# Kernel optimization log

Measured on AMD Instinct MI355X. Metric: run time of the kernel, lower is better.

Reference implementation:

```python
import jax, jax.numpy as jnp
import numpy as np

N = 100000      # nodes
E = 2500000     # edges
DIN, H, DOUT = 3, 32, 4
EPS = 1e-5

def _lin(k, i, o):
    kw, kb = jax.random.split(k)
    lim = 1.0 / np.sqrt(i)
    W = jax.random.uniform(kw, (i, o), jnp.float32, -lim, lim)
    b = jax.random.uniform(kb, (o,), jnp.float32, -lim, lim)
    return W, b

def setup_inputs():
    key = jax.random.key(0)
    ks = jax.random.split(key, 12)
    x = jax.random.normal(ks[0], (N, DIN), jnp.float32)
    edge_index = jax.random.randint(ks[1], (2, E), 0, N, dtype=jnp.int32)
    w_in1, b_in1 = _lin(ks[2], DIN, H)
    w_in2, b_in2 = _lin(ks[3], H, H)
    gamma = jnp.ones((H,), jnp.float32)
    beta = jnp.zeros((H,), jnp.float32)
    wg1, bg1 = _lin(ks[4], H, H)
    wg2, bg2 = _lin(ks[5], H, H)
    wg3, bg3 = _lin(ks[6], H, H)
    wo1, bo1 = _lin(ks[7], H, H)
    wo2, bo2 = _lin(ks[8], H, H)
    wo3, bo3 = _lin(ks[9], H, DOUT)
    return dict(x=x, w_in1=w_in1, b_in1=b_in1, w_in2=w_in2, b_in2=b_in2,
                gamma=gamma, beta=beta,
                wg1=wg1, bg1=bg1, wg2=wg2, bg2=bg2, wg3=wg3, bg3=bg3,
                wo1=wo1, bo1=bo1, wo2=wo2, bo2=bo2, wo3=wo3, bo3=bo3,
                edge_index=edge_index)

def _gcn(h, W, b, src, dst, norm):
    # PyG GCNConv: x' = scatter_add(norm * (xW)[src] -> dst) + bias
    hw = h @ W                                   # [N, H]
    msg = hw[src] * norm[:, None]                # [E+N, H] gather + scale
    out = jax.ops.segment_sum(msg, dst, num_segments=N)
    return out + b

def reference(x, w_in1, b_in1, w_in2, b_in2, gamma, beta,
              wg1, bg1, wg2, bg2, wg3, bg3,
              wo1, bo1, wo2, bo2, wo3, bo3, edge_index):
    leaky = lambda v: jax.nn.leaky_relu(v, 0.01)
    # input MLP
    h = leaky(x @ w_in1 + b_in1)
    h = leaky(h @ w_in2 + b_in2)
    # BatchNorm1d (training-mode batch statistics, biased variance)
    mu = jnp.mean(h, axis=0)
    var = jnp.mean((h - mu) ** 2, axis=0)
    h = (h - mu) * jax.lax.rsqrt(var + EPS) * gamma + beta
    # gcn_norm with self-loops: deg over target index, sym normalization
    loop = jnp.arange(N, dtype=edge_index.dtype)
    src = jnp.concatenate([edge_index[0], loop])
    dst = jnp.concatenate([edge_index[1], loop])
    deg = jax.ops.segment_sum(jnp.ones_like(src, jnp.float32), dst, num_segments=N)
    dis = jax.lax.rsqrt(deg)                     # deg >= 1 due to self-loops
    norm = dis[src] * dis[dst]                   # [E+N]
    h = jax.nn.elu(_gcn(h, wg1, bg1, src, dst, norm))
    h = jax.nn.elu(_gcn(h, wg2, bg2, src, dst, norm))
    h = jax.nn.elu(_gcn(h, wg3, bg3, src, dst, norm))
    # output MLP
    r = leaky(h @ wo1 + bo1)
    r = leaky(r @ wo2 + bo2)
    r = r @ wo3 + bo3                            # [N, 4]
    r = r.at[:, 0].set(jax.nn.sigmoid(r[:, 0]))
    return r
```

## Files before the change

kernel.cpp:

```cpp
#include <hip/hip_runtime.h>
#include <hip/hip_fp16.h>

#define HF 32
#define EPS 1e-5f
#define BSH 7
#define BSZ 128
#define CH  4096
#define SUBCAP 512
#define CAP (8*SUBCAP)

typedef int vi4 __attribute__((ext_vector_type(4)));

__device__ __forceinline__ float leaky(float v){ return fmaxf(v, 0.01f*v); }
__device__ __forceinline__ float elu1(float v){ return v > 0.f ? v : (expf(v)-1.f); }
__device__ __forceinline__ float sigmoidf(float v){ return 1.f/(1.f+expf(-v)); }

__device__ __forceinline__ int4 nt_load_i4(const int* p){
    vi4 v = __builtin_nontemporal_load((const vi4*)p);
    return make_int4(v.x, v.y, v.z, v.w);
}

__device__ __forceinline__ void addrow8(float* a, float4 v){
    const __half2* p = (const __half2*)&v;
#pragma unroll
    for (int k = 0; k < 4; k++){
        float2 f = __half22float2(p[k]);
        a[2*k] += f.x; a[2*k+1] += f.y;
    }
}
__device__ __forceinline__ float4 h2add4f(float4 a, float4 b){
    __half2* pa = (__half2*)&a; __half2* pb = (__half2*)&b;
    float4 r; __half2* pr = (__half2*)&r;
#pragma unroll
    for (int k = 0; k < 4; k++) pr[k] = __hadd2(pa[k], pb[k]);
    return r;
}

union SMem {
    struct {
        float sW1[3*HF]; float sB1[HF]; float sW2[HF*HF]; float sB2[HF];
        float sh[256][33];
    } mlp;
    struct { int lcnt[1024]; int lbase[1024]; int lpos[1024]; } bin;
};

__global__ __launch_bounds__(256)
void k_mlp_bin(const float* __restrict__ x,
               const float* __restrict__ w1, const float* __restrict__ b1,
               const float* __restrict__ w2, const float* __restrict__ b2,
               __half* __restrict__ h, float* __restrict__ stats,
               const int* __restrict__ src, const int* __restrict__ dst,
               int* __restrict__ gfill, int* __restrict__ ep,
               int N, int E, int B, int NC){
    __shared__ SMem sm;
    int t = threadIdx.x;
    if ((int)blockIdx.x < NC){
        int bid = blockIdx.x;
        for (int i = t; i < B; i += 256){ sm.bin.lcnt[i] = 0; sm.bin.lpos[i] = 0; }
        __syncthreads();
        int base = bid * CH;
        int xcd = bid & 7;
        int dv[16], sv[16];
        if (base + CH <= E){
#pragma unroll
            for (int i = 0; i < 4; i++){
                int4 d4 = nt_load_i4(dst + base + (t + i*256)*4);
                int4 s4 = nt_load_i4(src + base + (t + i*256)*4);
                dv[4*i]   = d4.x; dv[4*i+1] = d4.y; dv[4*i+2] = d4.z; dv[4*i+3] = d4.w;
                sv[4*i]   = s4.x; sv[4*i+1] = s4.y; sv[4*i+2] = s4.z; sv[4*i+3] = s4.w;
            }
        } else {
#pragma unroll
            for (int i = 0; i < 16; i++){
                int e = base + t + i*256;
                dv[i] = (e < E) ? dst[e] : -1;
                sv[i] = (e < E) ? src[e] : 0;
            }
        }
#pragma unroll
        for (int i = 0; i < 16; i++)
            if (dv[i] >= 0) atomicAdd(&sm.bin.lcnt[dv[i] >> BSH], 1);
        __syncthreads();
        for (int i = t; i < B; i += 256){
            int c = sm.bin.lcnt[i];
            sm.bin.lbase[i] = c ? (i*CAP + xcd*SUBCAP + atomicAdd(&gfill[i*8 + xcd], c)) : 0;
        }
        __syncthreads();
#pragma unroll
        for (int i = 0; i < 16; i++)
            if (dv[i] >= 0){
                int bb = dv[i] >> BSH;
                int p = sm.bin.lbase[bb] + atomicAdd(&sm.bin.lpos[bb], 1);
                ep[p] = (sv[i] << BSH) | (dv[i] & (BSZ-1));
            }
    } else {
        for (int i = t; i < 3*HF; i += 256) sm.mlp.sW1[i] = w1[i];
        if (t < HF){ sm.mlp.sB1[t] = b1[t]; sm.mlp.sB2[t] = b2[t]; }
        for (int i = t; i < HF*HF; i += 256) sm.mlp.sW2[i] = w2[i];
        __syncthreads();
        int n = (blockIdx.x - NC)*256 + t;
        float h2[HF];
        if (n < N){
            float x0 = x[(size_t)n*3], x1 = x[(size_t)n*3+1], x2 = x[(size_t)n*3+2];
            float h1[HF];
#pragma unroll
            for (int j = 0; j < HF; j++){
                float v = fmaf(x0, sm.mlp.sW1[j], fmaf(x1, sm.mlp.sW1[HF+j],
                          fmaf(x2, sm.mlp.sW1[2*HF+j], sm.mlp.sB1[j])));
                h1[j] = leaky(v);
            }
#pragma unroll
            for (int j = 0; j < HF; j++){
                float v = sm.mlp.sB2[j];
#pragma unroll
                for (int i = 0; i < HF; i++) v = fmaf(h1[i], sm.mlp.sW2[i*HF+j], v);
                h2[j] = leaky(v);
            }
            float4* hv = (float4*)(h + (size_t)n*HF);
#pragma unroll
            for (int jb = 0; jb < 4; jb++){
                __half2 hh[4];
#pragma unroll
                for (int k = 0; k < 4; k++)
                    hh[k] = __float22half2_rn(make_float2(h2[jb*8+2*k], h2[jb*8+2*k+1]));
                hv[jb] = *(float4*)hh;
            }
        } else {
#pragma unroll
            for (int j = 0; j < HF; j++) h2[j] = 0.f;
        }
#pragma unroll
        for (int j = 0; j < HF; j++) sm.mlp.sh[t][j] = h2[j];
        __syncthreads();
        int f = t & 31, g = t >> 5;
        float s = 0.f, ss = 0.f;
        for (int i = 0; i < 32; i++){
            float v = sm.mlp.sh[g*32 + i][f];
            s += v; ss += v*v;
        }
        __syncthreads();
        sm.mlp.sh[g][f] = s; sm.mlp.sh[8+g][f] = ss;
        __syncthreads();
        if (t < HF){
            float a = 0.f, b = 0.f;
#pragma unroll
            for (int g2 = 0; g2 < 8; g2++){ a += sm.mlp.sh[g2][t]; b += sm.mlp.sh[8+g2][t]; }
            atomicAdd(&stats[t], a);
            atomicAdd(&stats[HF+t], b);
        }
    }
}

__global__ __launch_bounds__(256)
void k_csr_t1(int* __restrict__ ep, const int* __restrict__ gfill,
              int2* __restrict__ rowp2, float* __restrict__ dis,
              int* __restrict__ norder,
              const __half* __restrict__ h, const float* __restrict__ stats,
              const float* __restrict__ gamma, const float* __restrict__ beta,
              const float* __restrict__ W, __half* __restrict__ tout,
              int N, int B){
    __shared__ int sep[CAP];
    __shared__ int lcnt[128], lpre[128], lfill[128];
    __shared__ float sW[HF*HF];
    __shared__ float sscale[HF], sshift[HF];
    int t = threadIdx.x;
    int b = blockIdx.x;
    for (int i = t; i < HF*HF; i += 256) sW[i] = W[i];
    if (t < HF){
        float inv = 1.0f/(float)N;
        float mu  = stats[t]*inv;
        float var = stats[HF+t]*inv - mu*mu;
        float rs  = rsqrtf(var + EPS);
        float sc  = rs*gamma[t];
        sscale[t] = sc;
        sshift[t] = beta[t] - mu*sc;
    }
    if (t < 128){ lcnt[t] = 0; lfill[t] = 0; }
    int cx[8], coff[8], cnt = 0;
#pragma unroll
    for (int xx = 0; xx < 8; xx++){ cx[xx] = gfill[b*8 + xx]; coff[xx] = cnt; cnt += cx[xx]; }
    int base = b*CAP;
    __syncthreads();
#pragma unroll
    for (int xx = 0; xx < 8; xx++)
        for (int j = t; j < cx[xx]; j += 256) sep[coff[xx] + j] = ep[base + xx*SUBCAP + j];
    __syncthreads();
    for (int e = t; e < cnt; e += 256) atomicAdd(&lcnt[sep[e] & (BSZ-1)], 1);
    __syncthreads();
    int dg = 0; float dloc = 0.f; int n = b*BSZ + t;
    if (t < 128){
        dg = lcnt[t];
        int pre = 0, rank = 0;
        for (int j = 0; j < 128; j++){
            int dj = lcnt[j];
            if (j < t) pre += dj;
            if (dj > dg || (dj == dg && j < t)) rank++;
        }
        lpre[t] = pre;
        if (n < N){
            rowp2[n] = make_int2(base + pre, base + pre + dg);
            dloc = rsqrtf((float)dg + 1.0f);
            dis[n] = dloc;
            norder[b*BSZ + rank] = n;
        } else {
            norder[b*BSZ + rank] = -1;
        }
    }
    __syncthreads();
    for (int e = t; e < cnt; e += 256){
        int val = sep[e];
        int d = val & (BSZ-1);
        int p = lpre[d] + atomicAdd(&lfill[d], 1);
        ep[base + p] = val >> BSH;
    }
    if (t < 128 && n < N){
        const float4* hv4 = (const float4*)h + (size_t)n*4;
        float v[HF];
#pragma unroll
        for (int k = 0; k < 4; k++){
            float4 raw = hv4[k];
            const __half2* p2 = (const __half2*)&raw;
#pragma unroll
            for (int q = 0; q < 4; q++){
                float2 f2 = __half22float2(p2[q]);
                v[8*k + 2*q]     = f2.x;
                v[8*k + 2*q + 1] = f2.y;
            }
        }
#pragma unroll
        for (int f = 0; f < HF; f++) v[f] = fmaf(v[f], sscale[f], sshift[f]);
        float o[HF];
#pragma unroll
        for (int j = 0; j < HF; j++) o[j] = 0.f;
#pragma unroll
        for (int i = 0; i < HF; i++){
            float vi = v[i];
#pragma unroll
            for (int j4 = 0; j4 < 8; j4++){
                float4 w4 = *(const float4*)&sW[i*HF + 4*j4];
                o[4*j4]   = fmaf(vi, w4.x, o[4*j4]);
                o[4*j4+1] = fmaf(vi, w4.y, o[4*j4+1]);
                o[4*j4+2] = fmaf(vi, w4.z, o[4*j4+2]);
                o[4*j4+3] = fmaf(vi, w4.w, o[4*j4+3]);
            }
        }
        float4* ov = (float4*)tout + (size_t)n*4;
#pragma unroll
        for (int k = 0; k < 4; k++){
            __half2 hh[4];
#pragma unroll
            for (int q = 0; q < 4; q++)
                hh[q] = __float22half2_rn(make_float2(o[8*k+2*q]*dloc, o[8*k+2*q+1]*dloc));
            ov[k] = *(float4*)hh;
        }
    }
}

__global__ __launch_bounds__(256)
void k_gather_t(const __half* __restrict__ tin, const int* __restrict__ esrc,
                const int2* __restrict__ rowp2, const float* __restrict__ dis,
                const int* __restrict__ norder,
                const float* __restrict__ bias, const float* __restrict__ W,
                __half* __restrict__ tout, int N){
    __shared__ float sW[HF*HF];
    __shared__ float sh[64][33];
    int tid = threadIdx.x;
    for (int i = tid; i < HF*HF; i += 256) sW[i] = W[i];
    int nib = tid >> 2, l = tid & 3;
    int n = norder[blockIdx.x*64 + nib];
    float acc[8] = {0.f,0.f,0.f,0.f,0.f,0.f,0.f,0.f};
    float d = 0.f;
    const float4* tv = (const float4*)tin;
    if (n >= 0){
        addrow8(acc, tv[(size_t)n*4 + l]);
        int2 r = rowp2[n];
        int e = r.x, e1 = r.y;
        while (e < e1 && (e & 3)){ addrow8(acc, tv[(size_t)esrc[e]*4 + l]); e++; }
        for (; e + 7 < e1; e += 8){
            int4 a4 = nt_load_i4(&esrc[e]);
            int4 b4 = nt_load_i4(&esrc[e+4]);
            float4 v0 = tv[(size_t)a4.x*4 + l];
            float4 v1 = tv[(size_t)a4.y*4 + l];
            float4 v2 = tv[(size_t)a4.z*4 + l];
            float4 v3 = tv[(size_t)a4.w*4 + l];
            float4 v4 = tv[(size_t)b4.x*4 + l];
            float4 v5 = tv[(size_t)b4.y*4 + l];
            float4 v6 = tv[(size_t)b4.z*4 + l];
            float4 v7 = tv[(size_t)b4.w*4 + l];
            addrow8(acc, h2add4f(h2add4f(v0, v1), h2add4f(v2, v3)));
            addrow8(acc, h2add4f(h2add4f(v4, v5), h2add4f(v6, v7)));
        }
        for (; e + 3 < e1; e += 4){
            int4 s4 = nt_load_i4(&esrc[e]);
            float4 v0 = tv[(size_t)s4.x*4 + l];
            float4 v1 = tv[(size_t)s4.y*4 + l];
            float4 v2 = tv[(size_t)s4.z*4 + l];
            float4 v3 = tv[(size_t)s4.w*4 + l];
            addrow8(acc, h2add4f(h2add4f(v0, v1), h2add4f(v2, v3)));
        }
        for (; e < e1; e++) addrow8(acc, tv[(size_t)esrc[e]*4 + l]);
        d = dis[n];
#pragma unroll
        for (int c = 0; c < 8; c++)
            acc[c] = elu1(fmaf(d, acc[c], bias[8*l + c]));
    }
    __syncthreads();
#pragma unroll
    for (int c = 0; c < 8; c++) sh[nib][8*l + c] = acc[c];
    __syncthreads();
    float o[8] = {0.f,0.f,0.f,0.f,0.f,0.f,0.f,0.f};
#pragma unroll
    for (int i = 0; i < HF; i++){
        float hvv = sh[nib][i];
        float4 w0 = *(const float4*)&sW[i*HF + 8*l];
        float4 w1 = *(const float4*)&sW[i*HF + 8*l + 4];
        o[0] = fmaf(hvv, w0.x, o[0]); o[1] = fmaf(hvv, w0.y, o[1]);
        o[2] = fmaf(hvv, w0.z, o[2]); o[3] = fmaf(hvv, w0.w, o[3]);
        o[4] = fmaf(hvv, w1.x, o[4]); o[5] = fmaf(hvv, w1.y, o[5]);
        o[6] = fmaf(hvv, w1.z, o[6]); o[7] = fmaf(hvv, w1.w, o[7]);
    }
    if (n >= 0){
        __half2 hh[4];
#pragma unroll
        for (int k = 0; k < 4; k++)
            hh[k] = __float22half2_rn(make_float2(o[2*k]*d, o[2*k+1]*d));
        ((float4*)tout)[(size_t)n*4 + l] = *(float4*)hh;
    }
}

__global__ __launch_bounds__(256)
void k_gather_out(const __half* __restrict__ tin, const int* __restrict__ esrc,
                  const int2* __restrict__ rowp2, const float* __restrict__ dis,
                  const int* __restrict__ norder,
                  const float* __restrict__ bg3,
                  const float* __restrict__ wo1, const float* __restrict__ bo1,
                  const float* __restrict__ wo2, const float* __restrict__ bo2,
                  const float* __restrict__ wo3, const float* __restrict__ bo3,
                  float* __restrict__ out, int N){
    __shared__ float sW1[HF*HF], sW2[HF*HF], sW3[HF*4];
    __shared__ float sh[64][33], sh2[64][33];
    int tid = threadIdx.x;
    for (int i = tid; i < HF*HF; i += 256){ sW1[i] = wo1[i]; sW2[i] = wo2[i]; }
    if (tid < HF*4) sW3[tid] = wo3[tid];
    int nib = tid >> 2, l = tid & 3;
    int n = norder[blockIdx.x*64 + nib];
    float acc[8] = {0.f,0.f,0.f,0.f,0.f,0.f,0.f,0.f};
    const float4* tv = (const float4*)tin;
    if (n >= 0){
        addrow8(acc, tv[(size_t)n*4 + l]);
        int2 r = rowp2[n];
        int e = r.x, e1 = r.y;
        while (e < e1 && (e & 3)){ addrow8(acc, tv[(size_t)esrc[e]*4 + l]); e++; }
        for (; e + 7 < e1; e += 8){
            int4 a4 = nt_load_i4(&esrc[e]);
            int4 b4 = nt_load_i4(&esrc[e+4]);
            float4 v0 = tv[(size_t)a4.x*4 + l];
            float4 v1 = tv[(size_t)a4.y*4 + l];
            float4 v2 = tv[(size_t)a4.z*4 + l];
            float4 v3 = tv[(size_t)a4.w*4 + l];
            float4 v4 = tv[(size_t)b4.x*4 + l];
            float4 v5 = tv[(size_t)b4.y*4 + l];
            float4 v6 = tv[(size_t)b4.z*4 + l];
            float4 v7 = tv[(size_t)b4.w*4 + l];
            addrow8(acc, h2add4f(h2add4f(v0, v1), h2add4f(v2, v3)));
            addrow8(acc, h2add4f(h2add4f(v4, v5), h2add4f(v6, v7)));
        }
        for (; e + 3 < e1; e += 4){
            int4 s4 = nt_load_i4(&esrc[e]);
            float4 v0 = tv[(size_t)s4.x*4 + l];
            float4 v1 = tv[(size_t)s4.y*4 + l];
            float4 v2 = tv[(size_t)s4.z*4 + l];
            float4 v3 = tv[(size_t)s4.w*4 + l];
            addrow8(acc, h2add4f(h2add4f(v0, v1), h2add4f(v2, v3)));
        }
        for (; e < e1; e++) addrow8(acc, tv[(size_t)esrc[e]*4 + l]);
        float d = dis[n];
#pragma unroll
        for (int c = 0; c < 8; c++)
            acc[c] = elu1(fmaf(d, acc[c], bg3[8*l + c]));
    }
    __syncthreads();
#pragma unroll
    for (int c = 0; c < 8; c++) sh[nib][8*l + c] = acc[c];
    __syncthreads();
    float o1[8];
#pragma unroll
    for (int c = 0; c < 8; c++) o1[c] = bo1[8*l + c];
#pragma unroll
    for (int i = 0; i < HF; i++){
        float hvv = sh[nib][i];
        float4 w0 = *(const float4*)&sW1[i*HF + 8*l];
        float4 w1 = *(const float4*)&sW1[i*HF + 8*l + 4];
        o1[0] = fmaf(hvv, w0.x, o1[0]); o1[1] = fmaf(hvv, w0.y, o1[1]);
        o1[2] = fmaf(hvv, w0.z, o1[2]); o1[3] = fmaf(hvv, w0.w, o1[3]);
        o1[4] = fmaf(hvv, w1.x, o1[4]); o1[5] = fmaf(hvv, w1.y, o1[5]);
        o1[6] = fmaf(hvv, w1.z, o1[6]); o1[7] = fmaf(hvv, w1.w, o1[7]);
    }
#pragma unroll
    for (int c = 0; c < 8; c++) sh2[nib][8*l + c] = leaky(o1[c]);
    __syncthreads();
    float o2[8];
#pragma unroll
    for (int c = 0; c < 8; c++) o2[c] = bo2[8*l + c];
#pragma unroll
    for (int i = 0; i < HF; i++){
        float hvv = sh2[nib][i];
        float4 w0 = *(const float4*)&sW2[i*HF + 8*l];
        float4 w1 = *(const float4*)&sW2[i*HF + 8*l + 4];
        o2[0] = fmaf(hvv, w0.x, o2[0]); o2[1] = fmaf(hvv, w0.y, o2[1]);
        o2[2] = fmaf(hvv, w0.z, o2[2]); o2[3] = fmaf(hvv, w0.w, o2[3]);
        o2[4] = fmaf(hvv, w1.x, o2[4]); o2[5] = fmaf(hvv, w1.y, o2[5]);
        o2[6] = fmaf(hvv, w1.z, o2[6]); o2[7] = fmaf(hvv, w1.w, o2[7]);
    }
#pragma unroll
    for (int c = 0; c < 8; c++) sh[nib][8*l + c] = leaky(o2[c]);
    __syncthreads();
    if (n >= 0){
        float v = bo3[l];
#pragma unroll
        for (int i = 0; i < HF; i++) v = fmaf(sh[nib][i], sW3[i*4 + l], v);
        if (l == 0) v = sigmoidf(v);
        out[(size_t)n*4 + l] = v;
    }
}

extern "C" void kernel_launch(void* const* d_in, const int* in_sizes, int n_in,
                              void* d_out, int out_size, void* d_ws, size_t ws_size,
                              hipStream_t stream) {
    const float* x     = (const float*)d_in[0];
    const float* w_in1 = (const float*)d_in[1];
    const float* b_in1 = (const float*)d_in[2];
    const float* w_in2 = (const float*)d_in[3];
    const float* b_in2 = (const float*)d_in[4];
    const float* gamma = (const float*)d_in[5];
    const float* beta  = (const float*)d_in[6];
    const float* wg1   = (const float*)d_in[7];
    const float* bg1   = (const float*)d_in[8];
    const float* wg2   = (const float*)d_in[9];
    const float* bg2   = (const float*)d_in[10];
    const float* wg3   = (const float*)d_in[11];
    const float* bg3   = (const float*)d_in[12];
    const float* wo1   = (const float*)d_in[13];
    const float* bo1   = (const float*)d_in[14];
    const float* wo2   = (const float*)d_in[15];
    const float* bo2   = (const float*)d_in[16];
    const float* wo3   = (const float*)d_in[17];
    const float* bo3   = (const float*)d_in[18];
    const int*   ei    = (const int*)d_in[19];

    int N = in_sizes[0] / 3;
    int E = in_sizes[19] / 2;
    int B = (N + BSZ - 1) >> BSH;

    char* w = (char*)d_ws;
    size_t o = 0;
    auto alloc = [&](size_t bytes){ size_t r = o; o = (o + bytes + 255) & ~(size_t)255; return r; };
    float* stats = (float*)(w + alloc(2*HF*sizeof(float)));
    int*   gfill = (int*)  (w + alloc((size_t)B*8*4));
    size_t zero_bytes = o;
    int2*  rowp2 = (int2*) (w + alloc((size_t)N*8));
    float* dis   = (float*)(w + alloc((size_t)N*4));
    int*   norder= (int*)  (w + alloc((size_t)B*BSZ*4));
    int*   ep    = (int*)  (w + alloc((size_t)B*CAP*4));
    __half* bufH = (__half*)(w + alloc((size_t)N*HF*2));
    __half* tA   = (__half*)(w + alloc((size_t)N*HF*2));
    __half* tB   = (__half*)(w + alloc((size_t)N*HF*2));

    hipMemsetAsync(d_ws, 0, zero_bytes, stream);

    const int* src = ei;
    const int* dst = ei + E;
    int NB1 = (N + 255) / 256;
    int NC  = (E + CH - 1) / CH;
    int NS  = 2*B;

    k_mlp_bin<<<NC + NB1, 256, 0, stream>>>(x, w_in1, b_in1, w_in2, b_in2, bufH, stats,
                                            src, dst, gfill, ep, N, E, B, NC);
    k_csr_t1<<<B, 256, 0, stream>>>(ep, gfill, rowp2, dis, norder,
                                    bufH, stats, gamma, beta, wg1, tA, N, B);
    k_gather_t<<<NS, 256, 0, stream>>>(tA, ep, rowp2, dis, norder, bg1, wg2, tB, N);
    k_gather_t<<<NS, 256, 0, stream>>>(tB, ep, rowp2, dis, norder, bg2, wg3, tA, N);
    k_gather_out<<<NS, 256, 0, stream>>>(tA, ep, rowp2, dis, norder, bg3,
                                         wo1, bo1, wo2, bo2, wo3, bo3, (float*)d_out, N);
}
```

Baseline: 307.4 us.

## Replace degree-sorted node ordering with 8 threads per node split across edge chunks

Removes the per-block degree ranking and norder permutation. The gather kernels now assign 8 threads per node (two halves of 4 lanes each take alternating 4-edge chunks) and combine them with a shuffle-xor reduction, halving nodes per block and doubling the grid. The dense transform work is also split so each lane computes 4 output features, and the first-layer transform in k_csr_t1 uses all 256 threads (two per node) instead of 128. This trades degree-sorted load balancing for more memory-level parallelism per node, but adds a shuffle reduction and an extra barrier.

```diff
diff --git a/kernel.cpp b/kernel.cpp
--- a/kernel.cpp
+++ b/kernel.cpp
@@ -154,7 +154,6 @@
 __global__ __launch_bounds__(256)
 void k_csr_t1(int* __restrict__ ep, const int* __restrict__ gfill,
               int2* __restrict__ rowp2, float* __restrict__ dis,
-              int* __restrict__ norder,
               const __half* __restrict__ h, const float* __restrict__ stats,
               const float* __restrict__ gamma, const float* __restrict__ beta,
               const float* __restrict__ W, __half* __restrict__ tout,
@@ -187,23 +186,15 @@
     __syncthreads();
     for (int e = t; e < cnt; e += 256) atomicAdd(&lcnt[sep[e] & (BSZ-1)], 1);
     __syncthreads();
-    int dg = 0; float dloc = 0.f; int n = b*BSZ + t;
     if (t < 128){
-        dg = lcnt[t];
-        int pre = 0, rank = 0;
-        for (int j = 0; j < 128; j++){
-            int dj = lcnt[j];
-            if (j < t) pre += dj;
-            if (dj > dg || (dj == dg && j < t)) rank++;
-        }
+        int dg = lcnt[t];
+        int pre = 0;
+        for (int j = 0; j < t; j++) pre += lcnt[j];
         lpre[t] = pre;
+        int n = b*BSZ + t;
         if (n < N){
             rowp2[n] = make_int2(base + pre, base + pre + dg);
-            dloc = rsqrtf((float)dg + 1.0f);
-            dis[n] = dloc;
-            norder[b*BSZ + rank] = n;
-        } else {
-            norder[b*BSZ + rank] = -1;
+            dis[n]   = rsqrtf((float)dg + 1.0f);
         }
     }
     __syncthreads();
@@ -213,7 +204,10 @@
         int p = lpre[d] + atomicAdd(&lfill[d], 1);
         ep[base + p] = val >> BSH;
     }
-    if (t < 128 && n < N){
+    int nloc = t >> 1, fh = (t & 1) * 16;
+    int n = b*BSZ + nloc;
+    if (n < N){
+        float dloc = rsqrtf((float)lcnt[nloc] + 1.0f);
         const float4* hv4 = (const float4*)h + (size_t)n*4;
         float v[HF];
 #pragma unroll
@@ -229,24 +223,24 @@
         }
 #pragma unroll
         for (int f = 0; f < HF; f++) v[f] = fmaf(v[f], sscale[f], sshift[f]);
-        float o[HF];
-#pragma unroll
-        for (int j = 0; j < HF; j++) o[j] = 0.f;
+        float o[16];
+#pragma unroll
+        for (int j = 0; j < 16; j++) o[j] = 0.f;
 #pragma unroll
         for (int i = 0; i < HF; i++){
             float vi = v[i];
 #pragma unroll
-            for (int j4 = 0; j4 < 8; j4++){
-                float4 w4 = *(const float4*)&sW[i*HF + 4*j4];
+            for (int j4 = 0; j4 < 4; j4++){
+                float4 w4 = *(const float4*)&sW[i*HF + fh + 4*j4];
                 o[4*j4]   = fmaf(vi, w4.x, o[4*j4]);
                 o[4*j4+1] = fmaf(vi, w4.y, o[4*j4+1]);
                 o[4*j4+2] = fmaf(vi, w4.z, o[4*j4+2]);
                 o[4*j4+3] = fmaf(vi, w4.w, o[4*j4+3]);
             }
         }
-        float4* ov = (float4*)tout + (size_t)n*4;
-#pragma unroll
-        for (int k = 0; k < 4; k++){
+        float4* ov = (float4*)tout + (size_t)n*4 + (t & 1)*2;
+#pragma unroll
+        for (int k = 0; k < 2; k++){
             __half2 hh[4];
 #pragma unroll
             for (int q = 0; q < 4; q++)
@@ -259,26 +253,28 @@
 __global__ __launch_bounds__(256)
 void k_gather_t(const __half* __restrict__ tin, const int* __restrict__ esrc,
                 const int2* __restrict__ rowp2, const float* __restrict__ dis,
-                const int* __restrict__ norder,
                 const float* __restrict__ bias, const float* __restrict__ W,
                 __half* __restrict__ tout, int N){
     __shared__ float sW[HF*HF];
-    __shared__ float sh[64][33];
+    __shared__ float sh[32][33];
     int tid = threadIdx.x;
     for (int i = tid; i < HF*HF; i += 256) sW[i] = W[i];
-    int nib = tid >> 2, l = tid & 3;
-    int n = norder[blockIdx.x*64 + nib];
+    int node = tid >> 3, l2 = tid & 7, l = l2 & 3, hf = l2 >> 2;
+    int n = blockIdx.x*32 + node;
     float acc[8] = {0.f,0.f,0.f,0.f,0.f,0.f,0.f,0.f};
     float d = 0.f;
     const float4* tv = (const float4*)tin;
-    if (n >= 0){
-        addrow8(acc, tv[(size_t)n*4 + l]);
+    if (n < N){
+        if (hf == 0) addrow8(acc, tv[(size_t)n*4 + l]);
         int2 r = rowp2[n];
-        int e = r.x, e1 = r.y;
-        while (e < e1 && (e & 3)){ addrow8(acc, tv[(size_t)esrc[e]*4 + l]); e++; }
-        for (; e + 7 < e1; e += 8){
-            int4 a4 = nt_load_i4(&esrc[e]);
-            int4 b4 = nt_load_i4(&esrc[e+4]);
+        int e0 = r.x, e1 = r.y;
+        int ea = (e0 + 3) & ~3; if (ea > e1) ea = e1;
+        if (hf == 0) for (int e = e0; e < ea; e++) addrow8(acc, tv[(size_t)esrc[e]*4 + l]);
+        int nch = (e1 - ea) >> 2;
+        int c = hf;
+        for (; c + 2 < nch; c += 4){
+            int4 a4 = nt_load_i4(&esrc[ea + 4*c]);
+            int4 b4 = nt_load_i4(&esrc[ea + 4*(c+2)]);
             float4 v0 = tv[(size_t)a4.x*4 + l];
             float4 v1 = tv[(size_t)a4.y*4 + l];
             float4 v2 = tv[(size_t)a4.z*4 + l];
@@ -290,70 +286,72 @@
             addrow8(acc, h2add4f(h2add4f(v0, v1), h2add4f(v2, v3)));
             addrow8(acc, h2add4f(h2add4f(v4, v5), h2add4f(v6, v7)));
         }
-        for (; e + 3 < e1; e += 4){
-            int4 s4 = nt_load_i4(&esrc[e]);
+        for (; c < nch; c += 2){
+            int4 s4 = nt_load_i4(&esrc[ea + 4*c]);
             float4 v0 = tv[(size_t)s4.x*4 + l];
             float4 v1 = tv[(size_t)s4.y*4 + l];
             float4 v2 = tv[(size_t)s4.z*4 + l];
             float4 v3 = tv[(size_t)s4.w*4 + l];
             addrow8(acc, h2add4f(h2add4f(v0, v1), h2add4f(v2, v3)));
         }
-        for (; e < e1; e++) addrow8(acc, tv[(size_t)esrc[e]*4 + l]);
+        if (hf == 1) for (int e = ea + 4*nch; e < e1; e++) addrow8(acc, tv[(size_t)esrc[e]*4 + l]);
+#pragma unroll
+        for (int cc = 0; cc < 8; cc++) acc[cc] += __shfl_xor(acc[cc], 4);
         d = dis[n];
 #pragma unroll
-        for (int c = 0; c < 8; c++)
-            acc[c] = elu1(fmaf(d, acc[c], bias[8*l + c]));
-    }
-    __syncthreads();
-#pragma unroll
-    for (int c = 0; c < 8; c++) sh[nib][8*l + c] = acc[c];
-    __syncthreads();
-    float o[8] = {0.f,0.f,0.f,0.f,0.f,0.f,0.f,0.f};
+        for (int cc = 0; cc < 8; cc++)
+            acc[cc] = elu1(fmaf(d, acc[cc], bias[8*l + cc]));
+    }
+    __syncthreads();
+    if (hf == 0){
+#pragma unroll
+        for (int cc = 0; cc < 8; cc++) sh[node][8*l + cc] = acc[cc];
+    }
+    __syncthreads();
+    float o[4] = {0.f,0.f,0.f,0.f};
 #pragma unroll
     for (int i = 0; i < HF; i++){
-        float hvv = sh[nib][i];
-        float4 w0 = *(const float4*)&sW[i*HF + 8*l];
-        float4 w1 = *(const float4*)&sW[i*HF + 8*l + 4];
-        o[0] = fmaf(hvv, w0.x, o[0]); o[1] = fmaf(hvv, w0.y, o[1]);
-        o[2] = fmaf(hvv, w0.z, o[2]); o[3] = fmaf(hvv, w0.w, o[3]);
-        o[4] = fmaf(hvv, w1.x, o[4]); o[5] = fmaf(hvv, w1.y, o[5]);
-        o[6] = fmaf(hvv, w1.z, o[6]); o[7] = fmaf(hvv, w1.w, o[7]);
-    }
-    if (n >= 0){
-        __half2 hh[4];
-#pragma unroll
-        for (int k = 0; k < 4; k++)
-            hh[k] = __float22half2_rn(make_float2(o[2*k]*d, o[2*k+1]*d));
-        ((float4*)tout)[(size_t)n*4 + l] = *(float4*)hh;
+        float hvv = sh[node][i];
+        float4 w4 = *(const float4*)&sW[i*HF + 4*l2];
+        o[0] = fmaf(hvv, w4.x, o[0]); o[1] = fmaf(hvv, w4.y, o[1]);
+        o[2] = fmaf(hvv, w4.z, o[2]); o[3] = fmaf(hvv, w4.w, o[3]);
+    }
+    if (n < N){
+        __half2 hh[2];
+        hh[0] = __float22half2_rn(make_float2(o[0]*d, o[1]*d));
+        hh[1] = __float22half2_rn(make_float2(o[2]*d, o[3]*d));
+        ((float2*)tout)[(size_t)n*8 + l2] = *(float2*)hh;
     }
 }
 
 __global__ __launch_bounds__(256)
 void k_gather_out(const __half* __restrict__ tin, const int* __restrict__ esrc,
                   const int2* __restrict__ rowp2, const float* __restrict__ dis,
-                  const int* __restrict__ norder,
                   const float* __restrict__ bg3,
                   const float* __restrict__ wo1, const float* __restrict__ bo1,
                   const float* __restrict__ wo2, const float* __restrict__ bo2,
                   const float* __restrict__ wo3, const float* __restrict__ bo3,
                   float* __restrict__ out, int N){
     __shared__ float sW1[HF*HF], sW2[HF*HF], sW3[HF*4];
-    __shared__ float sh[64][33], sh2[64][33];
+    __shared__ float sh[32][33], sh2[32][33];
     int tid = threadIdx.x;
     for (int i = tid; i < HF*HF; i += 256){ sW1[i] = wo1[i]; sW2[i] = wo2[i]; }
     if (tid < HF*4) sW3[tid] = wo3[tid];
-    int nib = tid >> 2, l = tid & 3;
-    int n = norder[blockIdx.x*64 + nib];
+    int node = tid >> 3, l2 = tid & 7, l = l2 & 3, hf = l2 >> 2;
+    int n = blockIdx.x*32 + node;
     float acc[8] = {0.f,0.f,0.f,0.f,0.f,0.f,0.f,0.f};
     const float4* tv = (const float4*)tin;
-    if (n >= 0){
-        addrow8(acc, tv[(size_t)n*4 + l]);
+    if (n < N){
+        if (hf == 0) addrow8(acc, tv[(size_t)n*4 + l]);
         int2 r = rowp2[n];
-        int e = r.x, e1 = r.y;
-        while (e < e1 && (e & 3)){ addrow8(acc, tv[(size_t)esrc[e]*4 + l]); e++; }
-        for (; e + 7 < e1; e += 8){
-            int4 a4 = nt_load_i4(&esrc[e]);
-            int4 b4 = nt_load_i4(&esrc[e+4]);
+        int e0 = r.x, e1 = r.y;
+        int ea = (e0 + 3) & ~3; if (ea > e1) ea = e1;
+        if (hf == 0) for (int e = e0; e < ea; e++) addrow8(acc, tv[(size_t)esrc[e]*4 + l]);
+        int nch = (e1 - ea) >> 2;
+        int c = hf;
+        for (; c + 2 < nch; c += 4){
+            int4 a4 = nt_load_i4(&esrc[ea + 4*c]);
+            int4 b4 = nt_load_i4(&esrc[ea + 4*(c+2)]);
             float4 v0 = tv[(size_t)a4.x*4 + l];
             float4 v1 = tv[(size_t)a4.y*4 + l];
             float4 v2 = tv[(size_t)a4.z*4 + l];
@@ -365,62 +363,61 @@
             addrow8(acc, h2add4f(h2add4f(v0, v1), h2add4f(v2, v3)));
             addrow8(acc, h2add4f(h2add4f(v4, v5), h2add4f(v6, v7)));
         }
-        for (; e + 3 < e1; e += 4){
-            int4 s4 = nt_load_i4(&esrc[e]);
+        for (; c < nch; c += 2){
+            int4 s4 = nt_load_i4(&esrc[ea + 4*c]);
             float4 v0 = tv[(size_t)s4.x*4 + l];
             float4 v1 = tv[(size_t)s4.y*4 + l];
             float4 v2 = tv[(size_t)s4.z*4 + l];
             float4 v3 = tv[(size_t)s4.w*4 + l];
             addrow8(acc, h2add4f(h2add4f(v0, v1), h2add4f(v2, v3)));
         }
-        for (; e < e1; e++) addrow8(acc, tv[(size_t)esrc[e]*4 + l]);
+        if (hf == 1) for (int e = ea + 4*nch; e < e1; e++) addrow8(acc, tv[(size_t)esrc[e]*4 + l]);
+#pragma unroll
+        for (int cc = 0; cc < 8; cc++) acc[cc] += __shfl_xor(acc[cc], 4);
         float d = dis[n];
 #pragma unroll
-        for (int c = 0; c < 8; c++)
-            acc[c] = elu1(fmaf(d, acc[c], bg3[8*l + c]));
-    }
-    __syncthreads();
-#pragma unroll
-    for (int c = 0; c < 8; c++) sh[nib][8*l + c] = acc[c];
-    __syncthreads();
-    float o1[8];
-#pragma unroll
-    for (int c = 0; c < 8; c++) o1[c] = bo1[8*l + c];
+        for (int cc = 0; cc < 8; cc++)
+            acc[cc] = elu1(fmaf(d, acc[cc], bg3[8*l + cc]));
+    }
+    __syncthreads();
+    if (hf == 0){
+#pragma unroll
+        for (int cc = 0; cc < 8; cc++) sh[node][8*l + cc] = acc[cc];
+    }
+    __syncthreads();
+    float o1[4];
+#pragma unroll
+    for (int cc = 0; cc < 4; cc++) o1[cc] = bo1[4*l2 + cc];
 #pragma unroll
     for (int i = 0; i < HF; i++){
-        float hvv = sh[nib][i];
-        float4 w0 = *(const float4*)&sW1[i*HF + 8*l];
-        float4 w1 = *(const float4*)&sW1[i*HF + 8*l + 4];
-        o1[0] = fmaf(hvv, w0.x, o1[0]); o1[1] = fmaf(hvv, w0.y, o1[1]);
-        o1[2] = fmaf(hvv, w0.z, o1[2]); o1[3] = fmaf(hvv, w0.w, o1[3]);
-        o1[4] = fmaf(hvv, w1.x, o1[4]); o1[5] = fmaf(hvv, w1.y, o1[5]);
-        o1[6] = fmaf(hvv, w1.z, o1[6]); o1[7] = fmaf(hvv, w1.w, o1[7]);
-    }
-#pragma unroll
-    for (int c = 0; c < 8; c++) sh2[nib][8*l + c] = leaky(o1[c]);
-    __syncthreads();
-    float o2[8];
-#pragma unroll
-    for (int c = 0; c < 8; c++) o2[c] = bo2[8*l + c];
+        float hvv = sh[node][i];
+        float4 w4 = *(const float4*)&sW1[i*HF + 4*l2];
+        o1[0] = fmaf(hvv, w4.x, o1[0]); o1[1] = fmaf(hvv, w4.y, o1[1]);
+        o1[2] = fmaf(hvv, w4.z, o1[2]); o1[3] = fmaf(hvv, w4.w, o1[3]);
+    }
+#pragma unroll
+    for (int cc = 0; cc < 4; cc++) sh2[node][4*l2 + cc] = leaky(o1[cc]);
+    __syncthreads();
+    float o2[4];
+#pragma unroll
+    for (int cc = 0; cc < 4; cc++) o2[cc] = bo2[4*l2 + cc];
 #pragma unroll
     for (int i = 0; i < HF; i++){
-        float hvv = sh2[nib][i];
-        float4 w0 = *(const float4*)&sW2[i*HF + 8*l];
-        float4 w1 = *(const float4*)&sW2[i*HF + 8*l + 4];
-        o2[0] = fmaf(hvv, w0.x, o2[0]); o2[1] = fmaf(hvv, w0.y, o2[1]);
-        o2[2] = fmaf(hvv, w0.z, o2[2]); o2[3] = fmaf(hvv, w0.w, o2[3]);
-        o2[4] = fmaf(hvv, w1.x, o2[4]); o2[5] = fmaf(hvv, w1.y, o2[5]);
-        o2[6] = fmaf(hvv, w1.z, o2[6]); o2[7] = fmaf(hvv, w1.w, o2[7]);
-    }
-#pragma unroll
-    for (int c = 0; c < 8; c++) sh[nib][8*l + c] = leaky(o2[c]);
-    __syncthreads();
-    if (n >= 0){
-        float v = bo3[l];
-#pragma unroll
-        for (int i = 0; i < HF; i++) v = fmaf(sh[nib][i], sW3[i*4 + l], v);
-        if (l == 0) v = sigmoidf(v);
-        out[(size_t)n*4 + l] = v;
+        float hvv = sh2[node][i];
+        float4 w4 = *(const float4*)&sW2[i*HF + 4*l2];
+        o2[0] = fmaf(hvv, w4.x, o2[0]); o2[1] = fmaf(hvv, w4.y, o2[1]);
+        o2[2] = fmaf(hvv, w4.z, o2[2]); o2[3] = fmaf(hvv, w4.w, o2[3]);
+    }
+    __syncthreads();
+#pragma unroll
+    for (int cc = 0; cc < 4; cc++) sh[node][4*l2 + cc] = leaky(o2[cc]);
+    __syncthreads();
+    if (n < N && l2 < 4){
+        float v = bo3[l2];
+#pragma unroll
+        for (int i = 0; i < HF; i++) v = fmaf(sh[node][i], sW3[i*4 + l2], v);
+        if (l2 == 0) v = sigmoidf(v);
+        out[(size_t)n*4 + l2] = v;
     }
 }
 
@@ -460,7 +457,6 @@
     size_t zero_bytes = o;
     int2*  rowp2 = (int2*) (w + alloc((size_t)N*8));
     float* dis   = (float*)(w + alloc((size_t)N*4));
-    int*   norder= (int*)  (w + alloc((size_t)B*BSZ*4));
     int*   ep    = (int*)  (w + alloc((size_t)B*CAP*4));
     __half* bufH = (__half*)(w + alloc((size_t)N*HF*2));
     __half* tA   = (__half*)(w + alloc((size_t)N*HF*2));
@@ -472,14 +468,14 @@
     const int* dst = ei + E;
     int NB1 = (N + 255) / 256;
     int NC  = (E + CH - 1) / CH;
-    int NS  = 2*B;
+    int GN  = (N + 31) / 32;
 
     k_mlp_bin<<<NC + NB1, 256, 0, stream>>>(x, w_in1, b_in1, w_in2, b_in2, bufH, stats,
                                             src, dst, gfill, ep, N, E, B, NC);
-    k_csr_t1<<<B, 256, 0, stream>>>(ep, gfill, rowp2, dis, norder,
+    k_csr_t1<<<B, 256, 0, stream>>>(ep, gfill, rowp2, dis,
                                     bufH, stats, gamma, beta, wg1, tA, N, B);
-    k_gather_t<<<NS, 256, 0, stream>>>(tA, ep, rowp2, dis, norder, bg1, wg2, tB, N);
-    k_gather_t<<<NS, 256, 0, stream>>>(tB, ep, rowp2, dis, norder, bg2, wg3, tA, N);
-    k_gather_out<<<NS, 256, 0, stream>>>(tA, ep, rowp2, dis, norder, bg3,
+    k_gather_t<<<GN, 256, 0, stream>>>(tA, ep, rowp2, dis, bg1, wg2, tB, N);
+    k_gather_t<<<GN, 256, 0, stream>>>(tB, ep, rowp2, dis, bg2, wg3, tA, N);
+    k_gather_out<<<GN, 256, 0, stream>>>(tA, ep, rowp2, dis, bg3,
                                          wo1, bo1, wo2, bo2, wo3, bo3, (float*)d_out, N);
 }
```

Result: faster. 286.4 us (-6.8%).
